# Performance work log

Hardware: AMD Instinct MI355X
Metric: run time of the kernel (lower is better)

The kernel has to match this reference:

```python
import jax, jax.numpy as jnp
import numpy as np

UNITS = 64
FEAT = 128
N_CLASSES = 10


def setup_inputs() -> dict:
    key = jax.random.key(0)
    ks = jax.random.split(key, 8)
    B, T, F = 512, 512, FEAT
    s_in = 1.0 / np.sqrt(F)
    s_rec = 1.0 / np.sqrt(UNITS)
    return {
        "inputs": jax.random.normal(ks[0], (B, T, F), dtype=jnp.float32),
        # GRU kernel [F, 3U], recurrent kernel [U, 3U], biases [2, 3U] (reset_after=True)
        "W": jax.random.normal(ks[1], (F, 3 * UNITS), dtype=jnp.float32) * s_in,
        "U": jax.random.normal(ks[2], (UNITS, 3 * UNITS), dtype=jnp.float32) * s_rec,
        "b": jnp.zeros((2, 3 * UNITS), dtype=jnp.float32),
        "W1": jax.random.normal(ks[3], (UNITS, 64), dtype=jnp.float32) * s_rec,
        "b1": jnp.zeros((64,), dtype=jnp.float32),
        "W2": jax.random.normal(ks[4], (64, N_CLASSES), dtype=jnp.float32) * s_rec,
        "b2": jnp.zeros((N_CLASSES,), dtype=jnp.float32),
    }


def _gru_last(inputs, W, U, b):
    # Keras GRU, reset_after=True, activation=relu, recurrent_activation=sigmoid.
    B = inputs.shape[0]
    # Precompute input projections for all timesteps: [T, B, 3U]
    x_proj = jnp.einsum('btf,fg->tbg', inputs, W) + b[0]
    b_rec = b[1]

    def step(h, xp):
        rec = h @ U + b_rec  # [B, 3U]
        xz, xr, xh = jnp.split(xp, 3, axis=-1)
        rz, rr, rh = jnp.split(rec, 3, axis=-1)
        z = jax.nn.sigmoid(xz + rz)
        r = jax.nn.sigmoid(xr + rr)
        hh = jax.nn.relu(xh + r * rh)
        h_new = z * h + (1.0 - z) * hh
        return h_new, None

    h0 = jnp.zeros((B, UNITS), dtype=inputs.dtype)
    h_last, _ = jax.lax.scan(step, h0, x_proj)
    return h_last


def reference(inputs, W, U, b, W1, b1, W2, b2):
    h = _gru_last(inputs, W, U, b)          # [B, 64]
    x = jax.nn.relu(h @ W1 + b1)            # [B, 64]
    logits = x @ W2 + b2                    # [B, 10]
    return jax.nn.softmax(logits, axis=-1)
```

## Files before the change

kernel.cpp:

```cpp
#include <hip/hip_runtime.h>


#define B_SZ   512
#define T_SZ   512
#define F_SZ   128
#define UN     64
#define G3     192
#define CHUNK  16
#define NCHUNK (T_SZ / CHUNK)
#define NCLS   10
#define GP     196

using short8 = __attribute__((ext_vector_type(8))) short;
using f32x4  = __attribute__((ext_vector_type(4))) float;
using h2     = __attribute__((ext_vector_type(2))) __fp16;
typedef unsigned int u32;

union S8 { short8 s; u32 u[4]; };
union HU { h2 h; u32 u; };

__device__ __forceinline__ u32 permb(u32 a, u32 b, u32 sel) {
    return __builtin_amdgcn_perm(a, b, sel);
}
__device__ __forceinline__ unsigned short f2bf_rn(float f) {
    u32 u = __float_as_uint(f);
    u32 r = u + 0x7FFFu + ((u >> 16) & 1u);
    return (unsigned short)(r >> 16);
}
__device__ __forceinline__ float bf2f(unsigned short s) {
    return __uint_as_float(((u32)s) << 16);
}
__device__ __forceinline__ float sigmoid_fast(float x) {
    float t = -1.44269504f * x;
    float e; asm("v_exp_f32 %0, %1" : "=v"(e) : "v"(t));
    float d = 1.0f + e;
    float r; asm("v_rcp_f32 %0, %1" : "=v"(r) : "v"(d));
    return r;
}
__device__ __forceinline__ void split_pair(float f0, float f1, u32 &hi, u32 &lo) {
    u32 u0 = __float_as_uint(f0) & 0xffff0000u;
    u32 u1 = __float_as_uint(f1) & 0xffff0000u;
    float l0 = f0 - __uint_as_float(u0);
    float l1 = f1 - __uint_as_float(u1);
    hi = permb(u1, u0, 0x07060302u);
    lo = permb(__float_as_uint(l1), __float_as_uint(l0), 0x07060302u);
}
__device__ __forceinline__ u32 f16bits(float f) {
    __fp16 x = (__fp16)f;
    return (u32)__builtin_bit_cast(unsigned short, x);
}
__device__ __forceinline__ u32 packf16(float f0, float f1) {
    return f16bits(f0) | (f16bits(f1) << 16);
}
__device__ __forceinline__ float dot2acc(u32 hp, u32 up, float acc) {
#if __has_builtin(__builtin_amdgcn_fdot2)
    HU a, b; a.u = hp; b.u = up;
    return __builtin_amdgcn_fdot2(a.h, b.h, acc, false);
#else
    HU a, b; a.u = hp; b.u = up;
    acc = fmaf((float)a.h[0], (float)b.h[0], acc);
    return fmaf((float)a.h[1], (float)b.h[1], acc);
#endif
}
#define WAVE_SYNC() asm volatile("s_waitcnt lgkmcnt(0)" ::: "memory")
#define MFMA16(A, B, C) __builtin_amdgcn_mfma_f32_16x16x32_bf16((A), (B), (C), 0, 0, 0)

__global__ __launch_bounds__(256, 1)
void gru_fused13(const float* __restrict__ inp,
                 const float* __restrict__ W,
                 const float* __restrict__ U,
                 const float* __restrict__ bias,
                 const float* __restrict__ W1,
                 const float* __restrict__ b1,
                 const float* __restrict__ W2,
                 const float* __restrict__ b2,
                 float* __restrict__ out)
{
    const int tid  = threadIdx.x;
    const int wv   = tid >> 6;
    const int lane = tid & 63;
    const int l15  = lane & 15;
    const int l4   = lane >> 4;
    const int r0   = blockIdx.x * 2;

    __shared__ __align__(16) float Xb[2][2][CHUNK][GP];
    __shared__ float hb[2][UN];
    __shared__ float sc[2][UN];
    __shared__ float lg[2][NCLS];

    if (wv >= 2) {
        const int tb = 6 * (wv - 2);
        short8 Wh[6][4], Wl[6][4];
        float  b0c[6];
        #pragma unroll
        for (int nt = 0; nt < 6; ++nt) {
            const int col = 16 * (tb + nt) + l15;
            b0c[nt] = bias[col];
            #pragma unroll
            for (int kt = 0; kt < 4; ++kt) {
                #pragma unroll
                for (int e = 0; e < 8; ++e) {
                    float w = W[(size_t)(32 * kt + 8 * l4 + e) * G3 + col];
                    unsigned short hi = f2bf_rn(w);
                    Wh[nt][kt][e] = (short)hi;
                    Wl[nt][kt][e] = (short)f2bf_rn(w - bf2f(hi));
                }
            }
        }

        auto produce = [&](int cn) {
            const int bn = cn & 1;
            #pragma unroll
            for (int r = 0; r < 2; ++r) {
                const float* ap = inp + (size_t)(r0 + r) * T_SZ * F_SZ
                                + (size_t)(cn * CHUNK + l15) * F_SZ + 8 * l4;
                f32x4 acc[6];
                #pragma unroll
                for (int nt = 0; nt < 6; ++nt) acc[nt] = (f32x4){0.f, 0.f, 0.f, 0.f};
                #pragma unroll
                for (int kt = 0; kt < 4; ++kt) {
                    f32x4 v0 = *(const f32x4*)(ap + 32 * kt);
                    f32x4 v1 = *(const f32x4*)(ap + 32 * kt + 4);
                    S8 Ah, Al;
                    split_pair(v0[0], v0[1], Ah.u[0], Al.u[0]);
                    split_pair(v0[2], v0[3], Ah.u[1], Al.u[1]);
                    split_pair(v1[0], v1[1], Ah.u[2], Al.u[2]);
                    split_pair(v1[2], v1[3], Ah.u[3], Al.u[3]);
                    #pragma unroll
                    for (int nt = 0; nt < 6; ++nt) {
                        acc[nt] = MFMA16(Ah.s, Wh[nt][kt], acc[nt]);
                        acc[nt] = MFMA16(Al.s, Wh[nt][kt], acc[nt]);
                        acc[nt] = MFMA16(Ah.s, Wl[nt][kt], acc[nt]);
                    }
                }
                #pragma unroll
                for (int nt = 0; nt < 6; ++nt) {
                    const int col = 16 * (tb + nt) + l15;
                    #pragma unroll
                    for (int q = 0; q < 4; ++q)
                        Xb[bn][r][4 * l4 + q][col] = acc[nt][q] + b0c[nt];
                }
            }
        };

        produce(0);
        __syncthreads();
        for (int c = 0; c < NCHUNK; ++c) {
            if (c + 1 < NCHUNK) produce(c + 1);
            __syncthreads();
        }
    } else {
        u32 uz2[32], ur2[32], uh2c[32];
        #pragma unroll
        for (int p = 0; p < 32; ++p) {
            uz2[p]  = packf16(U[(size_t)(2 * p) * G3 + lane],
                              U[(size_t)(2 * p + 1) * G3 + lane]);
            ur2[p]  = packf16(U[(size_t)(2 * p) * G3 + 64 + lane],
                              U[(size_t)(2 * p + 1) * G3 + 64 + lane]);
            uh2c[p] = packf16(U[(size_t)(2 * p) * G3 + 128 + lane],
                              U[(size_t)(2 * p + 1) * G3 + 128 + lane]);
        }
        const float brz = bias[G3 + lane];
        const float brr = bias[G3 + 64 + lane];
        const float brh = bias[G3 + 128 + lane];
        const int odd = lane & 1;
        float h = 0.f;

        __syncthreads();

        for (int c = 0; c < NCHUNK; ++c) {
            const int buf = c & 1;

            float xzv[CHUNK], xrv[CHUNK], xhv[CHUNK];
            #pragma unroll
            for (int s = 0; s < CHUNK; ++s) {
                xzv[s] = Xb[buf][wv][s][lane];
                xrv[s] = Xb[buf][wv][s][64 + lane];
                xhv[s] = Xb[buf][wv][s][128 + lane];
            }

            #pragma unroll
            for (int s = 0; s < CHUNK; ++s) {
                const u32 hu = f16bits(h);
                const u32 nb = (u32)__builtin_amdgcn_mov_dpp((int)hu, 0xB1, 0xF, 0xF, true);
                const u32 lo16 = odd ? nb : hu;
                const u32 hi16 = odd ? hu : nb;
                const u32 pk = lo16 | (hi16 << 16);

                u32 hs[32];
                #pragma unroll
                for (int p = 0; p < 16; ++p) {
                    hs[p]      = (u32)__builtin_amdgcn_readlane((int)pk, 2 * p);
                    hs[p + 16] = (u32)__builtin_amdgcn_readlane((int)pk, 2 * p + 32);
                }

                float az0 = brz + xzv[s], az1 = 0.f, az2 = 0.f, az3 = 0.f;
                float ar0 = brr + xrv[s], ar1 = 0.f, ar2 = 0.f, ar3 = 0.f;
                float ac0 = brh,          ac1 = 0.f, ac2 = 0.f, ac3 = 0.f;
                #pragma unroll
                for (int p = 0; p < 8; ++p) {
                    az0 = dot2acc(hs[p],      uz2[p],       az0);
                    az1 = dot2acc(hs[p + 8],  uz2[p + 8],   az1);
                    az2 = dot2acc(hs[p + 16], uz2[p + 16],  az2);
                    az3 = dot2acc(hs[p + 24], uz2[p + 24],  az3);
                    ar0 = dot2acc(hs[p],      ur2[p],       ar0);
                    ar1 = dot2acc(hs[p + 8],  ur2[p + 8],   ar1);
                    ar2 = dot2acc(hs[p + 16], ur2[p + 16],  ar2);
                    ar3 = dot2acc(hs[p + 24], ur2[p + 24],  ar3);
                    ac0 = dot2acc(hs[p],      uh2c[p],      ac0);
                    ac1 = dot2acc(hs[p + 8],  uh2c[p + 8],  ac1);
                    ac2 = dot2acc(hs[p + 16], uh2c[p + 16], ac2);
                    ac3 = dot2acc(hs[p + 24], uh2c[p + 24], ac3);
                }
                const float zpre = (az0 + az1) + (az2 + az3);
                const float rpre = (ar0 + ar1) + (ar2 + ar3);
                const float rh   = (ac0 + ac1) + (ac2 + ac3);
                const float z    = sigmoid_fast(zpre);
                const float rg   = sigmoid_fast(rpre);
                const float hh   = fmaxf(fmaf(rg, rh, xhv[s]), 0.f);
                h = fmaf(z, h - hh, hh);
            }
            __syncthreads();
        }

        hb[wv][lane] = h;
        WAVE_SYNC();

        float a = b1[lane];
        #pragma unroll 8
        for (int k = 0; k < UN; ++k)
            a = fmaf(hb[wv][k], W1[k * UN + lane], a);
        sc[wv][lane] = fmaxf(a, 0.f);
        WAVE_SYNC();

        if (lane < NCLS) {
            float acc = b2[lane];
            #pragma unroll 8
            for (int k = 0; k < UN; ++k)
                acc = fmaf(sc[wv][k], W2[k * NCLS + lane], acc);
            lg[wv][lane] = acc;
        }
        WAVE_SYNC();
        if (lane < NCLS) {
            float m = lg[wv][0];
            #pragma unroll
            for (int k = 1; k < NCLS; ++k) m = fmaxf(m, lg[wv][k]);
            float ss = 0.f;
            #pragma unroll
            for (int k = 0; k < NCLS; ++k) ss += __expf(lg[wv][k] - m);
            out[(r0 + wv) * NCLS + lane] = __expf(lg[wv][lane] - m) / ss;
        }
    }
}

extern "C" void kernel_launch(void* const* d_in, const int* in_sizes, int n_in,
                              void* d_out, int out_size, void* d_ws, size_t ws_size,
                              hipStream_t stream) {
    const float* inp  = (const float*)d_in[0];
    const float* W    = (const float*)d_in[1];
    const float* U    = (const float*)d_in[2];
    const float* bias = (const float*)d_in[3];
    const float* W1   = (const float*)d_in[4];
    const float* b1   = (const float*)d_in[5];
    const float* W2   = (const float*)d_in[6];
    const float* b2   = (const float*)d_in[7];
    float* out = (float*)d_out;

    gru_fused13<<<B_SZ / 2, 256, 0, stream>>>(inp, W, U, bias, W1, b1, W2, b2, out);
}
```

Measured before the change: 175.0 us.

## Use one block per batch row with six producer waves

```diff
diff --git a/kernel.cpp b/kernel.cpp
--- a/kernel.cpp
+++ b/kernel.cpp
@@ -65,8 +65,8 @@
 #define WAVE_SYNC() asm volatile("s_waitcnt lgkmcnt(0)" ::: "memory")
 #define MFMA16(A, B, C) __builtin_amdgcn_mfma_f32_16x16x32_bf16((A), (B), (C), 0, 0, 0)
 
-__global__ __launch_bounds__(256, 1)
-void gru_fused13(const float* __restrict__ inp,
+__global__ __launch_bounds__(448, 4)
+void gru_fused14(const float* __restrict__ inp,
                  const float* __restrict__ W,
                  const float* __restrict__ U,
                  const float* __restrict__ bias,
@@ -81,19 +81,19 @@
     const int lane = tid & 63;
     const int l15  = lane & 15;
     const int l4   = lane >> 4;
-    const int r0   = blockIdx.x * 2;
-
-    __shared__ __align__(16) float Xb[2][2][CHUNK][GP];
-    __shared__ float hb[2][UN];
-    __shared__ float sc[2][UN];
-    __shared__ float lg[2][NCLS];
-
-    if (wv >= 2) {
-        const int tb = 6 * (wv - 2);
-        short8 Wh[6][4], Wl[6][4];
-        float  b0c[6];
+    const int row  = blockIdx.x;
+
+    __shared__ __align__(16) float Xb[2][CHUNK][GP];
+    __shared__ float hb[UN];
+    __shared__ float sc[UN];
+    __shared__ float lg[NCLS];
+
+    if (wv != 0) {
+        const int tb = 2 * (wv - 1);
+        short8 Wh[2][4], Wl[2][4];
+        float  b0c[2];
         #pragma unroll
-        for (int nt = 0; nt < 6; ++nt) {
+        for (int nt = 0; nt < 2; ++nt) {
             const int col = 16 * (tb + nt) + l15;
             b0c[nt] = bias[col];
             #pragma unroll
@@ -110,36 +110,33 @@
 
         auto produce = [&](int cn) {
             const int bn = cn & 1;
-            #pragma unroll
-            for (int r = 0; r < 2; ++r) {
-                const float* ap = inp + (size_t)(r0 + r) * T_SZ * F_SZ
-                                + (size_t)(cn * CHUNK + l15) * F_SZ + 8 * l4;
-                f32x4 acc[6];
-                #pragma unroll
-                for (int nt = 0; nt < 6; ++nt) acc[nt] = (f32x4){0.f, 0.f, 0.f, 0.f};
-                #pragma unroll
-                for (int kt = 0; kt < 4; ++kt) {
-                    f32x4 v0 = *(const f32x4*)(ap + 32 * kt);
-                    f32x4 v1 = *(const f32x4*)(ap + 32 * kt + 4);
-                    S8 Ah, Al;
-                    split_pair(v0[0], v0[1], Ah.u[0], Al.u[0]);
-                    split_pair(v0[2], v0[3], Ah.u[1], Al.u[1]);
-                    split_pair(v1[0], v1[1], Ah.u[2], Al.u[2]);
-                    split_pair(v1[2], v1[3], Ah.u[3], Al.u[3]);
-                    #pragma unroll
-                    for (int nt = 0; nt < 6; ++nt) {
-                        acc[nt] = MFMA16(Ah.s, Wh[nt][kt], acc[nt]);
-                        acc[nt] = MFMA16(Al.s, Wh[nt][kt], acc[nt]);
-                        acc[nt] = MFMA16(Ah.s, Wl[nt][kt], acc[nt]);
-                    }
-                }
-                #pragma unroll
-                for (int nt = 0; nt < 6; ++nt) {
-                    const int col = 16 * (tb + nt) + l15;
-                    #pragma unroll
-                    for (int q = 0; q < 4; ++q)
-                        Xb[bn][r][4 * l4 + q][col] = acc[nt][q] + b0c[nt];
-                }
+            const float* ap = inp + (size_t)row * T_SZ * F_SZ
+                            + (size_t)(cn * CHUNK + l15) * F_SZ + 8 * l4;
+            f32x4 acc[2];
+            acc[0] = (f32x4){0.f, 0.f, 0.f, 0.f};
+            acc[1] = (f32x4){0.f, 0.f, 0.f, 0.f};
+            #pragma unroll
+            for (int kt = 0; kt < 4; ++kt) {
+                f32x4 v0 = *(const f32x4*)(ap + 32 * kt);
+                f32x4 v1 = *(const f32x4*)(ap + 32 * kt + 4);
+                S8 Ah, Al;
+                split_pair(v0[0], v0[1], Ah.u[0], Al.u[0]);
+                split_pair(v0[2], v0[3], Ah.u[1], Al.u[1]);
+                split_pair(v1[0], v1[1], Ah.u[2], Al.u[2]);
+                split_pair(v1[2], v1[3], Ah.u[3], Al.u[3]);
+                #pragma unroll
+                for (int nt = 0; nt < 2; ++nt) {
+                    acc[nt] = MFMA16(Ah.s, Wh[nt][kt], acc[nt]);
+                    acc[nt] = MFMA16(Al.s, Wh[nt][kt], acc[nt]);
+                    acc[nt] = MFMA16(Ah.s, Wl[nt][kt], acc[nt]);
+                }
+            }
+            #pragma unroll
+            for (int nt = 0; nt < 2; ++nt) {
+                const int col = 16 * (tb + nt) + l15;
+                #pragma unroll
+                for (int q = 0; q < 4; ++q)
+                    Xb[bn][4 * l4 + q][col] = acc[nt][q] + b0c[nt];
             }
         };
 
@@ -170,17 +167,12 @@
 
         for (int c = 0; c < NCHUNK; ++c) {
             const int buf = c & 1;
-
-            float xzv[CHUNK], xrv[CHUNK], xhv[CHUNK];
-            #pragma unroll
+            #pragma unroll 2
             for (int s = 0; s < CHUNK; ++s) {
-                xzv[s] = Xb[buf][wv][s][lane];
-                xrv[s] = Xb[buf][wv][s][64 + lane];
-                xhv[s] = Xb[buf][wv][s][128 + lane];
-            }
-
-            #pragma unroll
-            for (int s = 0; s < CHUNK; ++s) {
+                const float xz = Xb[buf][s][lane];
+                const float xr = Xb[buf][s][64 + lane];
+                const float xh = Xb[buf][s][128 + lane];
+
                 const u32 hu = f16bits(h);
                 const u32 nb = (u32)__builtin_amdgcn_mov_dpp((int)hu, 0xB1, 0xF, 0xF, true);
                 const u32 lo16 = odd ? nb : hu;
@@ -194,9 +186,9 @@
                     hs[p + 16] = (u32)__builtin_amdgcn_readlane((int)pk, 2 * p + 32);
                 }
 
-                float az0 = brz + xzv[s], az1 = 0.f, az2 = 0.f, az3 = 0.f;
-                float ar0 = brr + xrv[s], ar1 = 0.f, ar2 = 0.f, ar3 = 0.f;
-                float ac0 = brh,          ac1 = 0.f, ac2 = 0.f, ac3 = 0.f;
+                float az0 = brz + xz, az1 = 0.f, az2 = 0.f, az3 = 0.f;
+                float ar0 = brr + xr, ar1 = 0.f, ar2 = 0.f, ar3 = 0.f;
+                float ac0 = brh,      ac1 = 0.f, ac2 = 0.f, ac3 = 0.f;
                 #pragma unroll
                 for (int p = 0; p < 8; ++p) {
                     az0 = dot2acc(hs[p],      uz2[p],       az0);
@@ -217,38 +209,38 @@
                 const float rh   = (ac0 + ac1) + (ac2 + ac3);
                 const float z    = sigmoid_fast(zpre);
                 const float rg   = sigmoid_fast(rpre);
-                const float hh   = fmaxf(fmaf(rg, rh, xhv[s]), 0.f);
+                const float hh   = fmaxf(fmaf(rg, rh, xh), 0.f);
                 h = fmaf(z, h - hh, hh);
             }
             __syncthreads();
         }
 
-        hb[wv][lane] = h;
+        hb[lane] = h;
         WAVE_SYNC();
 
         float a = b1[lane];
         #pragma unroll 8
         for (int k = 0; k < UN; ++k)
-            a = fmaf(hb[wv][k], W1[k * UN + lane], a);
-        sc[wv][lane] = fmaxf(a, 0.f);
+            a = fmaf(hb[k], W1[k * UN + lane], a);
+        sc[lane] = fmaxf(a, 0.f);
         WAVE_SYNC();
 
         if (lane < NCLS) {
             float acc = b2[lane];
             #pragma unroll 8
             for (int k = 0; k < UN; ++k)
-                acc = fmaf(sc[wv][k], W2[k * NCLS + lane], acc);
-            lg[wv][lane] = acc;
+                acc = fmaf(sc[k], W2[k * NCLS + lane], acc);
+            lg[lane] = acc;
         }
         WAVE_SYNC();
         if (lane < NCLS) {
-            float m = lg[wv][0];
-            #pragma unroll
-            for (int k = 1; k < NCLS; ++k) m = fmaxf(m, lg[wv][k]);
+            float m = lg[0];
+            #pragma unroll
+            for (int k = 1; k < NCLS; ++k) m = fmaxf(m, lg[k]);
             float ss = 0.f;
             #pragma unroll
-            for (int k = 0; k < NCLS; ++k) ss += __expf(lg[wv][k] - m);
-            out[(r0 + wv) * NCLS + lane] = __expf(lg[wv][lane] - m) / ss;
+            for (int k = 0; k < NCLS; ++k) ss += __expf(lg[k] - m);
+            out[row * NCLS + lane] = __expf(lg[lane] - m) / ss;
         }
     }
 }
@@ -266,5 +258,5 @@
     const float* b2   = (const float*)d_in[7];
     float* out = (float*)d_out;
 
-    gru_fused13<<<B_SZ / 2, 256, 0, stream>>>(inp, W, U, bias, W1, b1, W2, b2, out);
-}
+    gru_fused14<<<B_SZ, 448, 0, stream>>>(inp, W, U, bias, W1, b1, W2, b2, out);
+}
```

Measured after the change: 217.9 us. +24.5%, slower.
